# Performance work log

Hardware: AMD Instinct MI355X
Metric: run time of the kernel (lower is better)

## Reference

```python
import jax, jax.numpy as jnp
import numpy as np

D_MODEL = 1024
D_INNER = 2048      # expand * d_model
D_STATE = 64
HEADDIM = 128
NHEADS = 16         # d_inner // headdim
D_CONV = 4
CHUNK = 256
D_IN_PROJ = 2 * D_INNER + 2 * D_STATE + NHEADS   # 4240 (ngroups=1)
CONV_DIM = D_INNER + 2 * D_STATE                 # 2176
EPS = 1e-5


def setup_inputs() -> dict:
    key = jax.random.key(0)
    ks = jax.random.split(key, 8)
    B, L = 2, 4096
    u = jax.random.normal(ks[0], (B, L, D_MODEL), jnp.float32)
    in_proj_w = jax.random.normal(ks[1], (D_IN_PROJ, D_MODEL), jnp.float32) / np.sqrt(D_MODEL)
    conv_w = jax.random.uniform(ks[2], (CONV_DIM, D_CONV), jnp.float32, -0.5, 0.5)
    conv_b = jnp.zeros((CONV_DIM,), jnp.float32)
    # dt_bias init exactly as in the module: inv-softplus of dt ~ logU(1e-3, 1e-1)
    dt0 = jnp.exp(jax.random.uniform(ks[3], (NHEADS,), jnp.float32) * (np.log(0.1) - np.log(0.001)) + np.log(0.001))
    dt_bias = dt0 + jnp.log(-jnp.expm1(-dt0))
    A_log = jnp.log(jax.random.uniform(ks[4], (NHEADS,), jnp.float32, 1.0, 16.0))
    Dp = jnp.ones((NHEADS,), jnp.float32)
    norm_w = jnp.ones((D_INNER,), jnp.float32)
    out_proj_w = jax.random.normal(ks[5], (D_MODEL, D_INNER), jnp.float32) / np.sqrt(D_INNER)
    return dict(u=u, in_proj_w=in_proj_w, conv_w=conv_w, conv_b=conv_b, dt_bias=dt_bias,
                A_log=A_log, Dp=Dp, norm_w=norm_w, out_proj_w=out_proj_w)


def _ssd(x, dt, A, Bm, Cm, Dp):
    # Chunked selective state-space scan (mamba_chunk_scan_combined semantics).
    # x: [b,l,h,p], dt: [b,l,h] (already softplus'd), A: [h] (negative), Bm/Cm: [b,l,n]
    b, l, h, p = x.shape
    n = Bm.shape[-1]
    nc = l // CHUNK
    xc = x.reshape(b, nc, CHUNK, h, p)
    dtc = dt.reshape(b, nc, CHUNK, h)
    Bc = Bm.reshape(b, nc, CHUNK, n)
    Cc = Cm.reshape(b, nc, CHUNK, n)
    a = dtc * A                       # [b,c,q,h], a <= 0
    acum = jnp.cumsum(a, axis=2)      # within-chunk cumulative log-decay
    # ---- intra-chunk (causal, attention-like) ----
    scores = jnp.einsum('bcqn,bckn->bcqk', Cc, Bc)
    diff = acum[:, :, :, None, :] - acum[:, :, None, :, :]        # [b,c,q,k,h]
    mask = jnp.tril(jnp.ones((CHUNK, CHUNK), bool))[None, None, :, :, None]
    decay = jnp.exp(jnp.where(mask, diff, -jnp.inf))
    M = scores[..., None] * decay * dtc[:, :, None, :, :]         # [b,c,q,k,h]
    y_diag = jnp.einsum('bcqkh,bckhp->bcqhp', M, xc)
    # ---- per-chunk end states ----
    decay_states = jnp.exp(acum[:, :, -1:, :] - acum)             # [b,c,q,h]
    states = jnp.einsum('bcqh,bcqn,bcqhp->bchpn', dtc * decay_states, Bc, xc)
    # ---- inter-chunk recurrence (scan over nc chunks) ----
    chunk_decay = jnp.exp(acum[:, :, -1, :])                      # [b,c,h]
    def step(s, inp):
        st, cd = inp
        return cd[:, :, None, None] * s + st, s                   # emit state BEFORE this chunk
    init = jnp.zeros((b, h, p, n), x.dtype)
    _, prev = jax.lax.scan(step, init, (states.transpose(1, 0, 2, 3, 4), chunk_decay.transpose(1, 0, 2)))
    prev = prev.transpose(1, 0, 2, 3, 4)                          # [b,c,h,p,n]
    y_off = jnp.einsum('bcqn,bchpn,bcqh->bcqhp', Cc, prev, jnp.exp(acum))
    y = y_diag + y_off + xc * Dp[None, None, None, :, None]
    return y.reshape(b, l, h, p)


def _forward(u, in_proj_w, conv_w, conv_b, dt_bias, A_log, Dp, norm_w, out_proj_w):
    b, l, _ = u.shape
    zxbct = jnp.einsum('bld,ed->ble', u, in_proj_w)
    z = zxbct[..., :D_INNER]
    xBC = zxbct[..., D_INNER:D_INNER + CONV_DIM]
    dt = zxbct[..., D_INNER + CONV_DIM:]
    dt = jax.nn.softplus(dt + dt_bias)                            # [b,l,h]
    # causal depthwise conv1d (padding d_conv-1, truncated to seq_len) + SiLU
    xp = jnp.pad(xBC, ((0, 0), (D_CONV - 1, 0), (0, 0)))
    conv_out = conv_b
    for w in range(D_CONV):
        conv_out = conv_out + xp[:, w:w + l, :] * conv_w[:, w]
    xBC = jax.nn.silu(conv_out)
    x = xBC[..., :D_INNER]
    Bm = xBC[..., D_INNER:D_INNER + D_STATE]
    Cm = xBC[..., D_INNER + D_STATE:]
    A = -jnp.exp(A_log)
    y = _ssd(x.reshape(b, l, NHEADS, HEADDIM), dt, A, Bm, Cm, Dp)
    y = y.reshape(b, l, D_INNER)
    # RMSNormGated (norm_before_gate=False): gate first, then RMSNorm
    y = y * jax.nn.silu(z)
    y = y * jax.lax.rsqrt(jnp.mean(y * y, axis=-1, keepdims=True) + EPS) * norm_w
    return jnp.einsum('ble,de->bld', y, out_proj_w)


def reference(u, in_proj_w, conv_w, conv_b, dt_bias, A_log, Dp, norm_w, out_proj_w):
    return _forward(u, in_proj_w, conv_w, conv_b, dt_bias, A_log, Dp, norm_w, out_proj_w)
```

## Files before the change

### kernel.cpp

```cpp
#include <hip/hip_runtime.h>
#include <hip/hip_bf16.h>
#include <cstdint>
#include <cstddef>

#define D_MODEL   1024
#define D_INNER   2048
#define D_STATE   64
#define HEADDIM   128
#define NHEADS    16
#define D_CONV    4
#define CHUNK     256
#define D_IN_PROJ 4240
#define ZPAD      4352
#define CONV_DIM  2176
#define NB        2
#define LEN       4096
#define NC        16
#define MROWS     (NB*LEN)

typedef __hip_bfloat16 bf16;
typedef __bf16 bf16x8 __attribute__((ext_vector_type(8)));
typedef float  f32x4  __attribute__((ext_vector_type(4)));
typedef unsigned short us4 __attribute__((ext_vector_type(4)));

__device__ __forceinline__ float fsilu(float x){ return x / (1.f + __expf(-x)); }
__device__ __forceinline__ float toF(float x){ return x; }
__device__ __forceinline__ float toF(bf16 x){ return __bfloat162float(x); }
__device__ __forceinline__ void storeF(float* p, float v){ *p = v; }
__device__ __forceinline__ void storeF(bf16* p, float v){ *p = __float2bfloat16(v); }

__device__ __forceinline__ unsigned short f2bs(float v){
  return __bfloat16_as_ushort(__float2bfloat16(v));
}
__device__ __forceinline__ void store4(bf16* p, f32x4 v){
  us4 o; o[0]=f2bs(v[0]); o[1]=f2bs(v[1]); o[2]=f2bs(v[2]); o[3]=f2bs(v[3]);
  *(us4*)p = o;
}
__device__ __forceinline__ void store4(float* p, f32x4 v){
  *(f32x4*)p = v;
}

__device__ __forceinline__ void gload_lds16(const void* g, void* l){
  __builtin_amdgcn_global_load_lds(
     (const __attribute__((address_space(1))) unsigned int*)(uintptr_t)g,
     (__attribute__((address_space(3))) unsigned int*)(uintptr_t)l, 16, 0, 0);
}

template<typename TC>
__global__ __launch_bounds__(256) void k_gemm_mfma(
    const bf16* __restrict__ A, int lda,
    const bf16* __restrict__ B, int ldb,
    TC* __restrict__ C, int ldc, int K)
{
  __shared__ __align__(16) bf16 As[2][128*32];
  __shared__ __align__(16) bf16 Bs[2][128*32];
  const int tid = threadIdx.x;
  const int w = tid >> 6, l = tid & 63;
  const int quad = l >> 4, lq = l & 15;
  const int m0 = blockIdx.x*128, n0 = blockIdx.y*128;
  const int wm = (w & 1)*64, wn = (w >> 1)*64;
  f32x4 acc[4][4] = {};
  const int sr = l >> 2;
  const int sc = (l & 3)*8;

  for (int k0 = 0; k0 < K; k0 += 64) {
    #pragma unroll
    for (int half = 0; half < 2; half++){
      #pragma unroll
      for (int j = 0; j < 2; j++) {
        const int blk = w*2 + j;
        const int row = blk*16 + sr;
        gload_lds16(A + (size_t)(m0+row)*lda + k0 + half*32 + sc, (char*)As[half] + blk*1024);
        gload_lds16(B + (size_t)(n0+row)*ldb + k0 + half*32 + sc, (char*)Bs[half] + blk*1024);
      }
    }
    asm volatile("s_waitcnt vmcnt(0)" ::: "memory");
    __syncthreads();

    const int kq = quad*8;
    #pragma unroll
    for (int half = 0; half < 2; half++){
      bf16x8 af[4], bfr[4];
      #pragma unroll
      for (int t = 0; t < 4; t++){
        af[t]  = *(const bf16x8*)&As[half][(wm + lq + t*16)*32 + kq];
        bfr[t] = *(const bf16x8*)&Bs[half][(wn + lq + t*16)*32 + kq];
      }
      #pragma unroll
      for (int tm = 0; tm < 4; tm++)
        #pragma unroll
        for (int tn = 0; tn < 4; tn++)
          acc[tm][tn] = __builtin_amdgcn_mfma_f32_16x16x32_bf16(bfr[tn], af[tm], acc[tm][tn], 0,0,0);
    }
    __syncthreads();
  }

  #pragma unroll
  for (int tm = 0; tm < 4; tm++){
    int r = m0 + wm + tm*16 + lq;
    #pragma unroll
    for (int tn = 0; tn < 4; tn++){
      int cb = n0 + wn + tn*16 + quad*4;
      store4(&C[(size_t)r*ldc + cb], acc[tm][tn]);
    }
  }
}

#define NU4  (MROWS*D_MODEL/4)
#define NW14 (ZPAD*D_MODEL/4)
#define NW24 (D_MODEL*D_INNER/4)
__global__ __launch_bounds__(256) void k_convert(
    const float* __restrict__ u, const float* __restrict__ Win,
    const float* __restrict__ Wout, const float* __restrict__ norm_w,
    bf16* __restrict__ ub, bf16* __restrict__ Wb_in, bf16* __restrict__ Wb_out){
  int i4 = blockIdx.x*256 + threadIdx.x;
  if (i4 < NU4){
    float4 v = ((const float4*)u)[i4];
    us4 o = {f2bs(v.x), f2bs(v.y), f2bs(v.z), f2bs(v.w)};
    ((us4*)ub)[i4] = o;
  } else if (i4 < NU4 + NW14){
    int j = i4 - NU4;
    int r = j >> 8;
    float4 v = make_float4(0.f,0.f,0.f,0.f);
    if (r < D_IN_PROJ) v = ((const float4*)Win)[j];
    us4 o = {f2bs(v.x), f2bs(v.y), f2bs(v.z), f2bs(v.w)};
    ((us4*)Wb_in)[j] = o;
  } else {
    int j = i4 - NU4 - NW14;
    float4 v = ((const float4*)Wout)[j];
    float4 nw = ((const float4*)norm_w)[j & 511];
    us4 o = {f2bs(v.x*nw.x), f2bs(v.y*nw.y), f2bs(v.z*nw.z), f2bs(v.w*nw.w)};
    ((us4*)Wb_out)[j] = o;
  }
}

__global__ __launch_bounds__(256) void k_dt(
    const bf16* __restrict__ zxbct, const float* __restrict__ dt_bias,
    const float* __restrict__ A_log, float* __restrict__ dt_t,
    float* __restrict__ acum_t, float* __restrict__ cd_t){
  int bid = blockIdx.x;
  int h = bid & 15, c = (bid>>4)&15, b = bid>>8;
  int q = threadIdx.x;
  size_t m = (size_t)(b*NC + c)*CHUNK + q;
  float x = toF(zxbct[m*ZPAD + (D_INNER + CONV_DIM) + h]) + dt_bias[h];
  float dtv = (x > 20.f) ? x : log1pf(__expf(x));
  float Ah = -__expf(A_log[h]);
  float a = dtv * Ah;
  __shared__ float sb[CHUNK];
  sb[q] = a;
  __syncthreads();
  #pragma unroll
  for (int off=1; off<CHUNK; off<<=1){
    float t = (q >= off) ? sb[q-off] : 0.f;
    __syncthreads();
    sb[q] += t;
    __syncthreads();
  }
  float ac = sb[q];
  size_t o = ((size_t)(b*NHEADS+h))*LEN + c*CHUNK + q;
  dt_t[o]   = dtv;
  acum_t[o] = ac;
  if (q == CHUNK-1) cd_t[(b*NHEADS+h)*NC + c] = __expf(ac);
}

__global__ __launch_bounds__(256) void k_conv(
    const bf16* __restrict__ zxbct, const float* __restrict__ conv_w,
    const float* __restrict__ conv_b, bf16* __restrict__ xbc){
  __shared__ __align__(16) __bf16 xs[67*64];
  __shared__ __align__(16) float  ws[64*4];
  __shared__ float bs[64];
  const int tid = threadIdx.x;
  const int cq = tid & 7;
  const int tm = tid >> 3;
  const int c0 = blockIdx.x*64;
  const int m0 = blockIdx.y*64;
  {
    int g = m0 - 3 + tm; if (g < 0) g = 0;
    *(bf16x8*)&xs[tm*64 + cq*8] =
        *(const bf16x8*)(zxbct + (size_t)g*ZPAD + D_INNER + c0 + cq*8);
    int g2 = m0 - 3 + tm + 32;
    *(bf16x8*)&xs[(tm+32)*64 + cq*8] =
        *(const bf16x8*)(zxbct + (size_t)g2*ZPAD + D_INNER + c0 + cq*8);
    if (tid < 24){
      int r3 = 64 + (tid >> 3);
      int g3 = m0 - 3 + r3;
      *(bf16x8*)&xs[r3*64 + cq*8] =
          *(const bf16x8*)(zxbct + (size_t)g3*ZPAD + D_INNER + c0 + cq*8);
    }
  }
  if (tid < 64)      *(float4*)&ws[tid*4] = *(const float4*)(conv_w + (size_t)(c0+tid)*4);
  else if (tid < 128) bs[tid-64] = conv_b[c0 + tid - 64];
  __syncthreads();

  #pragma unroll
  for (int rr=0; rr<2; rr++){
    const int r = tm + rr*32;
    const int m = m0 + r;
    const int l = m & (LEN-1);
    float acc[8];
    #pragma unroll
    for (int j=0;j<8;j++) acc[j] = bs[cq*8+j];
    #pragma unroll
    for (int w=0; w<D_CONV; w++){
      if (l - (D_CONV-1) + w >= 0){
        bf16x8 v = *(const bf16x8*)&xs[(r+w)*64 + cq*8];
        #pragma unroll
        for (int j=0;j<8;j++) acc[j] += (float)v[j] * ws[(cq*8+j)*4 + w];
      }
    }
    bf16x8 o;
    #pragma unroll
    for (int j=0;j<8;j++) o[j] = (__bf16)fsilu(acc[j]);
    *(bf16x8*)(xbc + (size_t)m*CONV_DIM + c0 + cq*8) = o;
  }
}

__global__ __launch_bounds__(256,2) void k_states(
    const bf16* __restrict__ xbc, const float* __restrict__ acum_t,
    const float* __restrict__ dt_t, float* __restrict__ states)
{
  const int bid = blockIdx.x;
  const int h = bid & 15, c = (bid>>4)&15, b = bid>>8;
  const int z = b*NC + c;
  const int tid = threadIdx.x;
  const int w = tid >> 6, l = tid & 63;
  const int quad = l >> 4, lq = l & 15;

  __shared__ __align__(16) __bf16 xsT[2][128*72];
  __shared__ __align__(16) __bf16 bts[2][64*72];

  const float* acum = acum_t + ((size_t)(b*NHEADS+h))*LEN + c*CHUNK;
  const float* dtc  = dt_t   + ((size_t)(b*NHEADS+h))*LEN + c*CHUNK;
  const float alast = acum[CHUNK-1];
  const bf16* xrow = xbc + (size_t)z*CHUNK*CONV_DIM + h*HEADDIM;
  const bf16* Brow = xbc + (size_t)z*CHUNK*CONV_DIM + D_INNER;

  f32x4 Sst[2][4] = {};

  auto stage = [&](int t, int buf){
    const int k0 = t*64;
    const bf16* xr = xrow + (size_t)(k0+l)*CONV_DIM;
    #pragma unroll
    for (int pass=0; pass<4; pass++){
      int pb = w*8 + pass*32;
      bf16x8 v = *(const bf16x8*)(xr + pb);
      #pragma unroll
      for (int j=0;j<8;j++) xsT[buf][(pb+j)*72 + l] = v[j];
    }
    float wl = dtc[k0+l] * __expf(alast - acum[k0+l]);
    const bf16* br = Brow + (size_t)(k0+l)*CONV_DIM;
    #pragma unroll
    for (int pass=0; pass<2; pass++){
      int nb = w*8 + pass*32;
      bf16x8 v = *(const bf16x8*)(br + nb);
      #pragma unroll
      for (int j=0;j<8;j++) bts[buf][(nb+j)*72 + l] = (__bf16)((float)v[j] * wl);
    }
  };

  stage(0, 0);
  for (int t = 0; t < 4; t++){
    const int buf = t & 1;
    __syncthreads();
    if (t < 3) stage(t+1, buf^1);
    #pragma unroll
    for (int s=0;s<2;s++){
      bf16x8 a2[2];
      #pragma unroll
      for (int mi=0;mi<2;mi++)
        a2[mi] = *(const bf16x8*)&xsT[buf][(w*32 + mi*16 + lq)*72 + s*32 + quad*8];
      #pragma unroll
      for (int ni=0;ni<4;ni++){
        bf16x8 bb = *(const bf16x8*)&bts[buf][(ni*16+lq)*72 + s*32 + quad*8];
        #pragma unroll
        for (int mi=0;mi<2;mi++)
          Sst[mi][ni] = __builtin_amdgcn_mfma_f32_16x16x32_bf16(bb, a2[mi], Sst[mi][ni], 0,0,0);
      }
    }
  }

  float* so = states + (size_t)bid*HEADDIM*D_STATE;
  #pragma unroll
  for (int mi=0;mi<2;mi++){
    int pp = w*32 + mi*16 + lq;
    #pragma unroll
    for (int ni=0;ni<4;ni++)
      store4(&so[pp*D_STATE + ni*16 + quad*4], Sst[mi][ni]);
  }
}

__global__ __launch_bounds__(256) void k_scan(
    const float* __restrict__ states, const float* __restrict__ cd_t,
    bf16* __restrict__ prevb){
  int b = blockIdx.x >> 4, h = blockIdx.x & 15;
  int pt = blockIdx.y;
  int tid = threadIdx.x;
  float carry[4] = {0.f,0.f,0.f,0.f};
  for (int c=0;c<NC;c++){
    size_t base = ((size_t)(b*256 + c*16 + h))*HEADDIM*D_STATE + (size_t)pt*1024;
    float cd = cd_t[(b*NHEADS+h)*NC + c];
    #pragma unroll
    for (int i=0;i<4;i++){
      size_t idx = base + (size_t)i*256 + tid;
      prevb[idx] = __float2bfloat16(carry[i]);
      carry[i] = carry[i]*cd + states[idx];
    }
  }
}

__global__ __launch_bounds__(256,2) void k_fused(
    const bf16* __restrict__ xbc, const float* __restrict__ acum_t,
    const float* __restrict__ dt_t, const float* __restrict__ Dp,
    const bf16* __restrict__ prevb, bf16* __restrict__ y)
{
  const int bid = blockIdx.x;
  const int h = bid & 15, c = (bid>>4)&15, b = bid>>8;
  const int z = b*NC + c;
  const int tid = threadIdx.x;
  const int w = tid >> 6, l = tid & 63;
  const int quad = l >> 4, lq = l & 15;

  __shared__ __align__(16) __bf16 xsT[2][128*72];
  __shared__ __align__(16) __bf16 Ms[4][32*40];
  __shared__ float acs[CHUNK], dts[CHUNK];

  const float* acum = acum_t + ((size_t)(b*NHEADS+h))*LEN + c*CHUNK;
  const float* dtc  = dt_t   + ((size_t)(b*NHEADS+h))*LEN + c*CHUNK;
  acs[tid] = acum[tid];
  dts[tid] = dtc[tid];

  const bf16* xrow = xbc + (size_t)z*CHUNK*CONV_DIM + h*HEADDIM;
  const bf16* Brow = xbc + (size_t)z*CHUNK*CONV_DIM + D_INNER;
  const bf16* Crow = xbc + (size_t)z*CHUNK*CONV_DIM + D_INNER + D_STATE;
  const bf16* pv   = prevb + (size_t)bid*HEADDIM*D_STATE;
  const float Dph = Dp[h];
  const int j0 = w, j1 = 7 - w;

  f32x4 Yacc[2][2][8] = {};

  auto stage = [&](int t, int buf){
    const bf16* xr = xrow + (size_t)(t*64+l)*CONV_DIM;
    #pragma unroll
    for (int pass=0; pass<4; pass++){
      int pb = w*8 + pass*32;
      bf16x8 v = *(const bf16x8*)(xr + pb);
      #pragma unroll
      for (int j=0;j<8;j++) xsT[buf][(pb+j)*72 + l] = v[j];
    }
  };

  stage(0, 0);
  __syncthreads();

  #pragma unroll
  for (int s=0;s<2;s++){
    bf16x8 bp[8];
    #pragma unroll
    for (int pn=0;pn<8;pn++)
      bp[pn] = *(const bf16x8*)(pv + (pn*16+lq)*D_STATE + s*32 + quad*8);
    #pragma unroll
    for (int half=0; half<2; half++){
      const int j = half ? j1 : j0;
      #pragma unroll
      for (int qm=0;qm<2;qm++){
        int row = j*32 + qm*16 + lq;
        float e = __expf(acs[row]);
        bf16x8 a = *(const bf16x8*)(Crow + (size_t)row*CONV_DIM + s*32 + quad*8);
        bf16x8 ae;
        #pragma unroll
        for (int jj=0;jj<8;jj++) ae[jj] = (__bf16)((float)a[jj] * e);
        #pragma unroll
        for (int pn=0;pn<8;pn++)
          Yacc[half][qm][pn] = __builtin_amdgcn_mfma_f32_16x16x32_bf16(bp[pn], ae, Yacc[half][qm][pn], 0,0,0);
      }
    }
  }

  for (int t = 0; t < 4; t++){
    const int buf = t & 1;
    if (t > 0) __syncthreads();
    if (t < 3) stage(t+1, buf^1);

    #pragma unroll
    for (int half=0; half<2; half++){
      const int j = half ? j1 : j0;
      if (2*t > j) continue;
      const int qbase = j*32;
      bf16x8 cf[2][2];
      #pragma unroll
      for (int s=0;s<2;s++)
        #pragma unroll
        for (int qm=0;qm<2;qm++)
          cf[s][qm] = *(const bf16x8*)(Crow + (size_t)(qbase+qm*16+lq)*CONV_DIM + s*32 + quad*8);
      #pragma unroll
      for (int kk=0; kk<2; kk++){
        const int kh = 2*t + kk;
        if (kh > j) continue;
        const int kb32  = kk*32;
        const int kbase = kh*32;
        f32x4 Sacc[2][2] = {};
        #pragma unroll
        for (int s=0;s<2;s++){
          bf16x8 bfk[2];
          #pragma unroll
          for (int kn=0;kn<2;kn++)
            bfk[kn] = *(const bf16x8*)(Brow + (size_t)(kbase+kn*16+lq)*CONV_DIM + s*32 + quad*8);
          #pragma unroll
          for (int kn=0;kn<2;kn++)
            #pragma unroll
            for (int qm=0;qm<2;qm++)
              Sacc[kn][qm] = __builtin_amdgcn_mfma_f32_16x16x32_bf16(bfk[kn], cf[s][qm], Sacc[kn][qm], 0,0,0);
        }
        #pragma unroll
        for (int qm=0;qm<2;qm++){
          int ql = qbase + qm*16 + lq;
          float aq = acs[ql];
          #pragma unroll
          for (int kn=0;kn<2;kn++){
            us4 o;
            #pragma unroll
            for (int i=0;i<4;i++){
              int kl = kbase + kn*16 + quad*4 + i;
              float v = Sacc[kn][qm][i] * __expf(aq - acs[kl]) * dts[kl];
              v = (kl < ql) ? v : ((kl == ql) ? v + Dph : 0.f);
              o[i] = f2bs(v);
            }
            *(us4*)&Ms[w][(qm*16+lq)*40 + kn*16 + quad*4] = o;
          }
        }
        asm volatile("s_waitcnt lgkmcnt(0)" ::: "memory");
        #pragma unroll
        for (int qm=0;qm<2;qm++){
          bf16x8 am = *(const bf16x8*)&Ms[w][(qm*16+lq)*40 + quad*8];
          #pragma unroll
          for (int pn=0;pn<8;pn++){
            bf16x8 bp = *(const bf16x8*)&xsT[buf][(pn*16+lq)*72 + kb32 + quad*8];
            Yacc[half][qm][pn] = __builtin_amdgcn_mfma_f32_16x16x32_bf16(bp, am, Yacc[half][qm][pn], 0,0,0);
          }
        }
      }
    }
  }

  bf16* yrow = y + (size_t)z*CHUNK*D_INNER + h*HEADDIM;
  #pragma unroll
  for (int half=0; half<2; half++){
    const int j = half ? j1 : j0;
    #pragma unroll
    for (int qm=0;qm<2;qm++){
      int q = j*32 + qm*16 + lq;
      #pragma unroll
      for (int pn=0;pn<8;pn++)
        store4(&yrow[(size_t)q*D_INNER + pn*16 + quad*4], Yacc[half][qm][pn]);
    }
  }
}

__global__ __launch_bounds__(256) void k_gatenorm(
    const bf16* __restrict__ zxbct, bf16* __restrict__ y){
  int m = blockIdx.x;
  int e0 = threadIdx.x*8;
  bf16x8 zv = *(const bf16x8*)(zxbct + (size_t)m*ZPAD + e0);
  bf16x8 yv = *(const bf16x8*)(y + (size_t)m*D_INNER + e0);
  float v[8]; float ss = 0.f;
  #pragma unroll
  for (int j=0;j<8;j++){
    float val = (float)yv[j] * fsilu((float)zv[j]);
    v[j] = val; ss += val*val;
  }
  #pragma unroll
  for (int off=32; off>0; off>>=1) ss += __shfl_down(ss, off, 64);
  __shared__ float red[4];
  if ((threadIdx.x & 63) == 0) red[threadIdx.x >> 6] = ss;
  __syncthreads();
  float tot = red[0]+red[1]+red[2]+red[3];
  float r = rsqrtf(tot * (1.f/D_INNER) + 1e-5f);
  bf16x8 o;
  #pragma unroll
  for (int j=0;j<8;j++) o[j] = (__bf16)(v[j] * r);
  *(bf16x8*)(y + (size_t)m*D_INNER + e0) = o;
}

extern "C" void kernel_launch(void* const* d_in, const int* in_sizes, int n_in,
                              void* d_out, int out_size, void* d_ws, size_t ws_size,
                              hipStream_t stream) {
  const float* u         = (const float*)d_in[0];
  const float* in_proj_w = (const float*)d_in[1];
  const float* conv_w    = (const float*)d_in[2];
  const float* conv_b    = (const float*)d_in[3];
  const float* dt_bias   = (const float*)d_in[4];
  const float* A_log     = (const float*)d_in[5];
  const float* Dp        = (const float*)d_in[6];
  const float* norm_w    = (const float*)d_in[7];
  const float* out_proj_w= (const float*)d_in[8];
  float* out = (float*)d_out;

  char* p = (char*)d_ws;
  auto alloc = [&](size_t bytes){ char* r = p; p += (bytes + 255) & ~size_t(255); return r; };
  bf16*  zxbct = (bf16*) alloc((size_t)MROWS*ZPAD*2);
  bf16*  xbc   = (bf16*) alloc((size_t)MROWS*CONV_DIM*2);
  bf16*  y     = (bf16*) alloc((size_t)MROWS*D_INNER*2);
  bf16*  ub    = (bf16*) alloc((size_t)MROWS*D_MODEL*2);
  bf16*  Wb_in = (bf16*) alloc((size_t)ZPAD*D_MODEL*2);
  bf16*  Wb_out= (bf16*) alloc((size_t)D_MODEL*D_INNER*2);
  float* dt_t  = (float*)alloc((size_t)NB*NHEADS*LEN*4);
  float* acum_t= (float*)alloc((size_t)NB*NHEADS*LEN*4);
  float* cd_t  = (float*)alloc((size_t)NB*NHEADS*NC*4);
  float* states= (float*)ub;
  bf16*  prevb = (bf16*)Wb_in;

  dim3 blk(256);
  k_convert<<<dim3((NU4+NW14+NW24)/256), blk, 0, stream>>>(
      u, in_proj_w, out_proj_w, norm_w, ub, Wb_in, Wb_out);

  k_gemm_mfma<bf16><<<dim3(MROWS/128, ZPAD/128), blk, 0, stream>>>(
      ub, D_MODEL, Wb_in, D_MODEL, zxbct, ZPAD, D_MODEL);

  k_dt    <<<dim3(NB*NC*NHEADS), blk, 0, stream>>>(zxbct, dt_bias, A_log, dt_t, acum_t, cd_t);
  k_conv  <<<dim3(CONV_DIM/64, MROWS/64), blk, 0, stream>>>(zxbct, conv_w, conv_b, xbc);
  k_states<<<dim3(NB*NC*NHEADS), blk, 0, stream>>>(xbc, acum_t, dt_t, states);
  k_scan  <<<dim3(NB*NHEADS, 8), blk, 0, stream>>>(states, cd_t, prevb);
  k_fused <<<dim3(NB*NC*NHEADS), blk, 0, stream>>>(xbc, acum_t, dt_t, Dp, prevb, y);
  k_gatenorm<<<dim3(MROWS), blk, 0, stream>>>(zxbct, y);

  k_gemm_mfma<float><<<dim3(MROWS/128, D_MODEL/128), blk, 0, stream>>>(
      y, D_INNER, Wb_out, D_INNER, out, D_MODEL, D_INNER);
}
```

Baseline: 363.6 us.

## Replace GEMM with triple-buffered 256x128-tile pipelined MFMA kernel

Rewrites the bf16 MFMA GEMM used for the in and out projections. It uses 512-thread blocks with 256x128 tiles, three LDS buffers that prefetch two k-steps ahead with partial vmcnt waits, XOR-swizzled LDS layout to avoid bank conflicts, and a workgroup remap for L2 locality. Both projection launches switch to a 1D grid. The aim is to hide global-load latency behind MFMA work and raise reuse per block. In exchange it needs 144KB of LDS per block, which limits occupancy to one block per CU, and the grid mapping hardcodes 32 M tiles.

```diff
diff --git a/kernel.cpp b/kernel.cpp
--- a/kernel.cpp
+++ b/kernel.cpp
@@ -47,61 +47,91 @@
 }
 
 template<typename TC>
-__global__ __launch_bounds__(256) void k_gemm_mfma(
+__global__ __launch_bounds__(512) void k_gemm_pipe(
     const bf16* __restrict__ A, int lda,
     const bf16* __restrict__ B, int ldb,
     TC* __restrict__ C, int ldc, int K)
 {
-  __shared__ __align__(16) bf16 As[2][128*32];
-  __shared__ __align__(16) bf16 Bs[2][128*32];
-  const int tid = threadIdx.x;
-  const int w = tid >> 6, l = tid & 63;
+  __shared__ __align__(16) char lds[3*49152];
+  const int tid  = threadIdx.x;
+  const int w    = tid >> 6, l = tid & 63;
   const int quad = l >> 4, lq = l & 15;
-  const int m0 = blockIdx.x*128, n0 = blockIdx.y*128;
-  const int wm = (w & 1)*64, wn = (w >> 1)*64;
+  const int wm   = w >> 1, wn = w & 1;
+
+  const int nwg  = gridDim.x;
+  const int orig = blockIdx.x;
+  const int wg   = (orig & 7)*(nwg >> 3) + (orig >> 3);
+  const int m0   = (wg & 31)*256;
+  const int n0   = (wg >> 5)*128;
+
+  const int rs = tid >> 3;
+  const int cs = ((tid & 7) ^ (rs & 7)) * 8;
+  const bf16* Ag = A + (size_t)(m0 + rs)*lda + cs;
+  const bf16* Bg = B + (size_t)(n0 + rs)*ldb + cs;
+  const int sdo = w*1024;
+
+  auto stage = [&](int k0, char* bufb){
+    #pragma unroll
+    for (int p=0;p<4;p++)
+      gload_lds16(Ag + (size_t)p*64*lda + k0, bufb + sdo + p*8192);
+    #pragma unroll
+    for (int p=0;p<2;p++)
+      gload_lds16(Bg + (size_t)p*64*ldb + k0, bufb + 32768 + sdo + p*8192);
+  };
+
+  char* bufA = lds;
+  char* bufB = lds + 49152;
+  char* bufC = lds + 98304;
+
   f32x4 acc[4][4] = {};
-  const int sr = l >> 2;
-  const int sc = (l & 3)*8;
-
-  for (int k0 = 0; k0 < K; k0 += 64) {
-    #pragma unroll
-    for (int half = 0; half < 2; half++){
-      #pragma unroll
-      for (int j = 0; j < 2; j++) {
-        const int blk = w*2 + j;
-        const int row = blk*16 + sr;
-        gload_lds16(A + (size_t)(m0+row)*lda + k0 + half*32 + sc, (char*)As[half] + blk*1024);
-        gload_lds16(B + (size_t)(n0+row)*ldb + k0 + half*32 + sc, (char*)Bs[half] + blk*1024);
-      }
-    }
-    asm volatile("s_waitcnt vmcnt(0)" ::: "memory");
-    __syncthreads();
-
-    const int kq = quad*8;
-    #pragma unroll
-    for (int half = 0; half < 2; half++){
-      bf16x8 af[4], bfr[4];
-      #pragma unroll
-      for (int t = 0; t < 4; t++){
-        af[t]  = *(const bf16x8*)&As[half][(wm + lq + t*16)*32 + kq];
-        bfr[t] = *(const bf16x8*)&Bs[half][(wn + lq + t*16)*32 + kq];
-      }
-      #pragma unroll
-      for (int tm = 0; tm < 4; tm++)
-        #pragma unroll
-        for (int tn = 0; tn < 4; tn++)
-          acc[tm][tn] = __builtin_amdgcn_mfma_f32_16x16x32_bf16(bfr[tn], af[tm], acc[tm][tn], 0,0,0);
-    }
-    __syncthreads();
-  }
-
-  #pragma unroll
-  for (int tm = 0; tm < 4; tm++){
-    int r = m0 + wm + tm*16 + lq;
-    #pragma unroll
-    for (int tn = 0; tn < 4; tn++){
-      int cb = n0 + wn + tn*16 + quad*4;
-      store4(&C[(size_t)r*ldc + cb], acc[tm][tn]);
+  const int sl0 = (quad ^ (lq & 7)) * 16;
+  const int sl1 = sl0 ^ 64;
+  const int aro = (wm*64 + lq)*128;
+  const int bro = 32768 + (wn*64 + lq)*128;
+
+  stage(0,  bufA);
+  stage(64, bufB);
+  asm volatile("s_waitcnt vmcnt(6)" ::: "memory");
+  __builtin_amdgcn_s_barrier();
+  asm volatile("" ::: "memory");
+
+  const int NT = K >> 6;
+  for (int t = 0; t < NT; ++t){
+    if (t + 2 < NT) stage((t+2) << 6, bufC);
+
+    bf16x8 af[2][4], bfr[2][4];
+    #pragma unroll
+    for (int m=0;m<4;m++){
+      af[0][m]  = *(const bf16x8*)(bufA + aro + m*2048 + sl0);
+      af[1][m]  = *(const bf16x8*)(bufA + aro + m*2048 + sl1);
+      bfr[0][m] = *(const bf16x8*)(bufA + bro + m*2048 + sl0);
+      bfr[1][m] = *(const bf16x8*)(bufA + bro + m*2048 + sl1);
+    }
+    __builtin_amdgcn_s_setprio(1);
+    #pragma unroll
+    for (int ks=0;ks<2;ks++)
+      #pragma unroll
+      for (int m=0;m<4;m++)
+        #pragma unroll
+        for (int n=0;n<4;n++)
+          acc[m][n] = __builtin_amdgcn_mfma_f32_16x16x32_bf16(bfr[ks][n], af[ks][m], acc[m][n], 0,0,0);
+    __builtin_amdgcn_s_setprio(0);
+
+    __builtin_amdgcn_sched_barrier(0);
+    if (t == NT-2) { asm volatile("s_waitcnt vmcnt(0)" ::: "memory"); }
+    else           { asm volatile("s_waitcnt vmcnt(6)" ::: "memory"); }
+    __builtin_amdgcn_s_barrier();
+    asm volatile("" ::: "memory");
+    char* tmp = bufA; bufA = bufB; bufB = bufC; bufC = tmp;
+  }
+
+  #pragma unroll
+  for (int m=0;m<4;m++){
+    const int r = m0 + wm*64 + m*16 + lq;
+    #pragma unroll
+    for (int n=0;n<4;n++){
+      const int cb = n0 + wn*64 + n*16 + quad*4;
+      store4(&C[(size_t)r*ldc + cb], acc[m][n]);
     }
   }
 }
@@ -513,7 +543,7 @@
   k_convert<<<dim3((NU4+NW14+NW24)/256), blk, 0, stream>>>(
       u, in_proj_w, out_proj_w, norm_w, ub, Wb_in, Wb_out);
 
-  k_gemm_mfma<bf16><<<dim3(MROWS/128, ZPAD/128), blk, 0, stream>>>(
+  k_gemm_pipe<bf16><<<dim3(32*34), dim3(512), 0, stream>>>(
       ub, D_MODEL, Wb_in, D_MODEL, zxbct, ZPAD, D_MODEL);
 
   k_dt    <<<dim3(NB*NC*NHEADS), blk, 0, stream>>>(zxbct, dt_bias, A_log, dt_t, acum_t, cd_t);
@@ -523,6 +553,6 @@
   k_fused <<<dim3(NB*NC*NHEADS), blk, 0, stream>>>(xbc, acum_t, dt_t, Dp, prevb, y);
   k_gatenorm<<<dim3(MROWS), blk, 0, stream>>>(zxbct, y);
 
-  k_gemm_mfma<float><<<dim3(MROWS/128, D_MODEL/128), blk, 0, stream>>>(
+  k_gemm_pipe<float><<<dim3(32*8), dim3(512), 0, stream>>>(
       y, D_INNER, Wb_out, D_INNER, out, D_MODEL, D_INNER);
 }
```

Result: slower. 386.1 us (+6.2%).

## Double-buffer GEMM shared-memory tiles and XOR-swizzle LDS layout

Applied to the files above, without the earlier changes.

Rewrites the MFMA GEMM so the next K-tile's global-to-LDS loads are issued before computing the current tile. It waits only on the older loads (vmcnt(8)), which overlaps memory latency with MFMA work. The LDS layout becomes 64-wide rows with an XOR swizzle on the 16-byte column slot, meant to reduce bank conflicts on fragment reads. The shared-memory footprint doubles to 64KB per block, which may lower occupancy.

```diff
diff --git a/kernel.cpp b/kernel.cpp
--- a/kernel.cpp
+++ b/kernel.cpp
@@ -26,8 +26,6 @@
 __device__ __forceinline__ float fsilu(float x){ return x / (1.f + __expf(-x)); }
 __device__ __forceinline__ float toF(float x){ return x; }
 __device__ __forceinline__ float toF(bf16 x){ return __bfloat162float(x); }
-__device__ __forceinline__ void storeF(float* p, float v){ *p = v; }
-__device__ __forceinline__ void storeF(bf16* p, float v){ *p = __float2bfloat16(v); }
 
 __device__ __forceinline__ unsigned short f2bs(float v){
   return __bfloat16_as_ushort(__float2bfloat16(v));
@@ -47,52 +45,66 @@
 }
 
 template<typename TC>
-__global__ __launch_bounds__(256) void k_gemm_mfma(
+__global__ __launch_bounds__(256) void k_gemm_db(
     const bf16* __restrict__ A, int lda,
     const bf16* __restrict__ B, int ldb,
     TC* __restrict__ C, int ldc, int K)
 {
-  __shared__ __align__(16) bf16 As[2][128*32];
-  __shared__ __align__(16) bf16 Bs[2][128*32];
-  const int tid = threadIdx.x;
-  const int w = tid >> 6, l = tid & 63;
+  __shared__ __align__(16) __bf16 As[2][128*64];
+  __shared__ __align__(16) __bf16 Bs[2][128*64];
+  const int tid  = threadIdx.x;
+  const int w    = tid >> 6, l = tid & 63;
   const int quad = l >> 4, lq = l & 15;
+  const int wm   = (w & 1)*64, wn = (w >> 1)*64;
   const int m0 = blockIdx.x*128, n0 = blockIdx.y*128;
-  const int wm = (w & 1)*64, wn = (w >> 1)*64;
+
+  const int rs = w*8 + (l >> 3);
+  const int cs = ((l & 7) ^ (l >> 3)) * 8;
+  const bf16* Ag = A + (size_t)(m0 + rs)*lda + cs;
+  const bf16* Bg = B + (size_t)(n0 + rs)*ldb + cs;
+
+  auto stage = [&](int t, int buf){
+    const int k0 = t*64;
+    #pragma unroll
+    for (int j=0;j<4;j++){
+      gload_lds16(Ag + (size_t)j*32*lda + k0, (char*)&As[buf][0] + (j*32 + w*8)*128);
+      gload_lds16(Bg + (size_t)j*32*ldb + k0, (char*)&Bs[buf][0] + (j*32 + w*8)*128);
+    }
+  };
+
   f32x4 acc[4][4] = {};
-  const int sr = l >> 2;
-  const int sc = (l & 3)*8;
-
-  for (int k0 = 0; k0 < K; k0 += 64) {
-    #pragma unroll
-    for (int half = 0; half < 2; half++){
-      #pragma unroll
-      for (int j = 0; j < 2; j++) {
-        const int blk = w*2 + j;
-        const int row = blk*16 + sr;
-        gload_lds16(A + (size_t)(m0+row)*lda + k0 + half*32 + sc, (char*)As[half] + blk*1024);
-        gload_lds16(B + (size_t)(n0+row)*ldb + k0 + half*32 + sc, (char*)Bs[half] + blk*1024);
-      }
-    }
-    asm volatile("s_waitcnt vmcnt(0)" ::: "memory");
-    __syncthreads();
-
-    const int kq = quad*8;
-    #pragma unroll
-    for (int half = 0; half < 2; half++){
+
+  stage(0, 0);
+  const int NT = K >> 6;
+  for (int t = 0; t < NT; ++t){
+    const int cur = t & 1;
+    if (t+1 < NT){
+      stage(t+1, cur^1);
+      asm volatile("s_waitcnt vmcnt(8)" ::: "memory");
+    } else {
+      asm volatile("s_waitcnt vmcnt(0)" ::: "memory");
+    }
+    asm volatile("s_barrier" ::: "memory");
+
+    const char* Ab = (const char*)&As[cur][0];
+    const char* Bb = (const char*)&Bs[cur][0];
+    #pragma unroll
+    for (int s=0;s<2;s++){
+      const int slot = ((s*4 + quad) ^ (lq & 7)) << 4;
       bf16x8 af[4], bfr[4];
       #pragma unroll
-      for (int t = 0; t < 4; t++){
-        af[t]  = *(const bf16x8*)&As[half][(wm + lq + t*16)*32 + kq];
-        bfr[t] = *(const bf16x8*)&Bs[half][(wn + lq + t*16)*32 + kq];
-      }
-      #pragma unroll
-      for (int tm = 0; tm < 4; tm++)
-        #pragma unroll
-        for (int tn = 0; tn < 4; tn++)
+      for (int tm=0;tm<4;tm++)
+        af[tm]  = *(const bf16x8*)(Ab + (wm + lq + tm*16)*128 + slot);
+      #pragma unroll
+      for (int tn=0;tn<4;tn++)
+        bfr[tn] = *(const bf16x8*)(Bb + (wn + lq + tn*16)*128 + slot);
+      #pragma unroll
+      for (int tm=0;tm<4;tm++)
+        #pragma unroll
+        for (int tn=0;tn<4;tn++)
           acc[tm][tn] = __builtin_amdgcn_mfma_f32_16x16x32_bf16(bfr[tn], af[tm], acc[tm][tn], 0,0,0);
     }
-    __syncthreads();
+    asm volatile("s_barrier" ::: "memory");
   }
 
   #pragma unroll
@@ -513,7 +525,7 @@
   k_convert<<<dim3((NU4+NW14+NW24)/256), blk, 0, stream>>>(
       u, in_proj_w, out_proj_w, norm_w, ub, Wb_in, Wb_out);
 
-  k_gemm_mfma<bf16><<<dim3(MROWS/128, ZPAD/128), blk, 0, stream>>>(
+  k_gemm_db<bf16><<<dim3(64, 34), blk, 0, stream>>>(
       ub, D_MODEL, Wb_in, D_MODEL, zxbct, ZPAD, D_MODEL);
 
   k_dt    <<<dim3(NB*NC*NHEADS), blk, 0, stream>>>(zxbct, dt_bias, A_log, dt_t, acum_t, cd_t);
@@ -523,6 +535,6 @@
   k_fused <<<dim3(NB*NC*NHEADS), blk, 0, stream>>>(xbc, acum_t, dt_t, Dp, prevb, y);
   k_gatenorm<<<dim3(MROWS), blk, 0, stream>>>(zxbct, y);
 
-  k_gemm_mfma<float><<<dim3(MROWS/128, D_MODEL/128), blk, 0, stream>>>(
+  k_gemm_db<float><<<dim3(64, 8), blk, 0, stream>>>(
       y, D_INNER, Wb_out, D_INNER, out, D_MODEL, D_INNER);
 }
```

Measured after the change: 344.4 us. 5.3% less time.
